# Performance work log

Measured on AMD Instinct MI355X. Metric: run time of the kernel, lower is better.

## Reference

```python
import jax, jax.numpy as jnp
import numpy as np
import math

B, CF, H, W = 2, 64, 256, 256
CH = 32          # 'channel' init arg
KS, DIL, PAD = 3, 2, 2
IMG_H, IMG_W = 512, 512


def _pos_encode(h, w, d_model):
    # Sinusoidal encoding along x and y, interleaved sin/cos -> [2*d_model, h, w]
    div = jnp.exp(jnp.arange(0, d_model, 2, dtype=jnp.float32) * (-math.log(10000.0) / d_model))  # [d/2]
    ax = jnp.arange(w, dtype=jnp.float32)[None, :] * div[:, None]   # [d/2, w]
    ay = jnp.arange(h, dtype=jnp.float32)[None, :] * div[:, None]   # [d/2, h]
    x = jnp.stack([jnp.sin(ax), jnp.cos(ax)], axis=1).reshape(d_model, w)  # even=sin, odd=cos
    y = jnp.stack([jnp.sin(ay), jnp.cos(ay)], axis=1).reshape(d_model, h)
    x = jnp.broadcast_to(x[:, None, :], (d_model, h, w))
    y = jnp.broadcast_to(y[:, :, None], (d_model, h, w))
    return jnp.concatenate([x, y], axis=0)  # [2*d_model, h, w]


def _unfold3x3(x):
    # F.unfold(kernel=3, dilation=2, padding=2, stride=1) -> [B, C, 9, H, W]
    b, c, h, w = x.shape
    xp = jnp.pad(x, ((0, 0), (0, 0), (PAD, PAD), (PAD, PAD)))
    offs = (0, DIL, 2 * DIL)
    patches = [xp[:, :, i:i + h, j:j + w] for i in offs for j in offs]  # row-major kernel order
    return jnp.stack(patches, axis=2)


def setup_inputs() -> dict:
    key = jax.random.key(0)
    k1, k2, k3, k4, k5 = jax.random.split(key, 5)
    return {
        "inp": jax.random.normal(k1, (B, CF, H, W), dtype=jnp.float32),
        "img": jax.random.uniform(k2, (B, 3, IMG_H, IMG_W), dtype=jnp.float32),
        "w_pos": jax.random.normal(k3, (CH, 2 * CH), dtype=jnp.float32) * 0.1,
        "w_img": jax.random.normal(k4, (CH, 3), dtype=jnp.float32) * 0.1,
        "w_comp": jax.random.normal(k5, (CF,), dtype=jnp.float32) * 0.1,
    }


def reference(inp, img, w_pos, w_img, w_comp):
    b, cf, h, w = inp.shape
    # positional embedding -> 1x1 conv (channel matmul)
    pos = _pos_encode(h, w, CH)                                   # [2*CH, H, W]
    pos_embd = jnp.einsum('oc,chw->ohw', w_pos, pos)              # [CH, H, W]
    pos_embd = jnp.broadcast_to(pos_embd[None], (b, CH, h, w))
    # bilinear resize of image to feature resolution, then 1x1 conv
    rimg = jax.image.resize(img, (b, 3, h, w), method='bilinear')
    rimg = jnp.einsum('oc,bchw->bohw', w_img, rimg)               # [B, CH, H, W]
    em = jnp.concatenate([rimg, pos_embd], axis=1)                # [B, 2*CH, H, W]
    # neighborhood similarity score
    un_em = _unfold3x3(em)                                        # [B, 2CH, 9, H, W]
    feature_score = jnp.einsum('bckhw,bchw->bkhw', un_em, em)     # [B, 9, H, W]
    # feature compatibility: 1x1 conv (dot with w_comp) per neighbor, sigmoid
    un_fea = _unfold3x3(inp)                                      # [B, CF, 9, H, W]
    comp_score = jax.nn.sigmoid(jnp.einsum('bckhw,c->bkhw', un_fea, w_comp))
    phi = comp_score * feature_score                              # [B, 9, H, W]
    weighted_fea = jnp.einsum('bckhw,bkhw->bchw', un_fea, phi)    # [B, CF, H, W]
    return weighted_fea
```

## Files before the change

kernel.cpp:

```cpp
#include <hip/hip_runtime.h>
#include <math.h>

namespace {
constexpr int Bn = 2, CF = 64;
constexpr int H = 256, W = 256, HW = H * W;
constexpr int IH = 512, IW = 512;

constexpr int OFF_MT   = 0;
constexpr int OFF_GXX  = OFF_MT + 256 * 256;
constexpr int OFF_GYY  = OFF_GXX + 3 * 256;
constexpr int OFF_G    = OFF_GYY + 3 * 256;
constexpr int OFF_RIMG = OFF_G + 16;
constexpr int OFF_S    = OFF_RIMG + Bn * 3 * HW;
constexpr int OFF_PHI  = OFF_S + Bn * HW;
constexpr int OFF_PX   = OFF_RIMG;
constexpr int OFF_PY   = OFF_RIMG + 32 * 256;
}

__global__ __launch_bounds__(256) void pxy_kernel(
    const float* __restrict__ w_pos,
    float* __restrict__ PX, float* __restrict__ PY)
{
  const int t = threadIdx.x;
  const int o = blockIdx.x;
  float s[16], c[16];
#pragma unroll
  for (int i = 0; i < 16; i++) {
    float d = expf((float)(2 * i) * (-0.2878231366242557f));
    float a = (float)t * d;
    s[i] = sinf(a);
    c[i] = cosf(a);
  }
  const float* wr = w_pos + o * 64;
  float ax = 0.f, ay = 0.f;
#pragma unroll
  for (int i = 0; i < 16; i++) {
    ax += wr[2 * i] * s[i] + wr[2 * i + 1] * c[i];
    ay += wr[32 + 2 * i] * s[i] + wr[33 + 2 * i] * c[i];
  }
  PX[o * 256 + t] = ax;
  PY[o * 256 + t] = ay;
}

__global__ __launch_bounds__(256) void gram_kernel(
    const float* __restrict__ PX, const float* __restrict__ PY,
    const float* __restrict__ w_img,
    float* __restrict__ Mt, float* __restrict__ GXX, float* __restrict__ GYY,
    float* __restrict__ G)
{
  const int a = threadIdx.x;
  const int t = blockIdx.x;

  float m = 0.f;
#pragma unroll
  for (int o = 0; o < 32; o++) m += PX[o * 256 + a] * PY[o * 256 + t];
  Mt[t * 256 + a] = m;

  if (t == 0) {
#pragma unroll
    for (int j = 0; j < 3; j++) {
      const int nb = a + 2 * (j - 1);
      float gx = 0.f, gy = 0.f;
      if (nb >= 0 && nb < 256) {
#pragma unroll
        for (int o = 0; o < 32; o++) {
          gx += PX[o * 256 + a] * PX[o * 256 + nb];
          gy += PY[o * 256 + a] * PY[o * 256 + nb];
        }
      }
      GXX[j * 256 + a] = gx;
      GYY[j * 256 + a] = gy;
    }
    if (a < 9) {
      const int i = a / 3, j = a % 3;
      float g = 0.f;
#pragma unroll
      for (int o = 0; o < 32; o++) g += w_img[o * 3 + i] * w_img[o * 3 + j];
      G[a] = g;
    }
  }
}

__device__ __forceinline__ void resize_taps(int p, int n, float w[4], int idx[4])
{
#pragma unroll
  for (int r = 0; r < 4; r++) {
    int q = 2 * p - 1 + r;
    idx[r] = min(max(q, 0), 2 * n - 1);
  }
  if (p == 0)          { w[0] = 0.f;        w[1] = 3.f / 7.f; w[2] = 3.f / 7.f; w[3] = 1.f / 7.f; }
  else if (p == n - 1) { w[0] = 1.f / 7.f;  w[1] = 3.f / 7.f; w[2] = 3.f / 7.f; w[3] = 0.f; }
  else                 { w[0] = 0.125f;     w[1] = 0.375f;    w[2] = 0.375f;    w[3] = 0.125f; }
}

__global__ __launch_bounds__(256) void rimg_kernel(
    const float* __restrict__ img, float* __restrict__ rimg)
{
  const int p = blockIdx.x * 256 + threadIdx.x;
  const int c = blockIdx.y;
  const int b = blockIdx.z;
  const int x = p & (W - 1);
  const int y = p >> 8;

  float wy[4], wx[4];
  int ry[4], rx[4];
  resize_taps(y, H, wy, ry);
  resize_taps(x, W, wx, rx);

  const float* ip = img + ((size_t)(b * 3 + c) * IH) * IW;
  float acc = 0.f;
#pragma unroll
  for (int r = 0; r < 4; r++) {
    const float* rowp = ip + ry[r] * IW;
    float rs = wx[0] * rowp[rx[0]] + wx[1] * rowp[rx[1]] +
               wx[2] * rowp[rx[2]] + wx[3] * rowp[rx[3]];
    acc += wy[r] * rs;
  }
  rimg[((size_t)(b * 3 + c)) * HW + p] = acc;
}

__global__ __launch_bounds__(256) void sigs_kernel(
    const float* __restrict__ inp, const float* __restrict__ w_comp,
    float* __restrict__ sigs)
{
  __shared__ float4 red[256];
  const int lane = threadIdx.x & 63;
  const int cg = threadIdx.x >> 6;
  const int p0 = blockIdx.x * 256 + lane * 4;
  const int b = blockIdx.z;

  const float* ib = inp + (size_t)b * CF * HW + (size_t)cg * 16 * HW + p0;
  float4 acc = {0.f, 0.f, 0.f, 0.f};
#pragma unroll
  for (int c = 0; c < 16; c++) {
    const float4 v = *reinterpret_cast<const float4*>(ib + (size_t)c * HW);
    const float wc = w_comp[cg * 16 + c];
    acc.x += v.x * wc; acc.y += v.y * wc;
    acc.z += v.z * wc; acc.w += v.w * wc;
  }
  red[threadIdx.x] = acc;
  __syncthreads();
  if (threadIdx.x < 64) {
    const float4 a = red[threadIdx.x];
    const float4 b1 = red[threadIdx.x + 64];
    const float4 c1 = red[threadIdx.x + 128];
    const float4 d = red[threadIdx.x + 192];
    float4 s;
    s.x = (a.x + b1.x) + (c1.x + d.x);
    s.y = (a.y + b1.y) + (c1.y + d.y);
    s.z = (a.z + b1.z) + (c1.z + d.z);
    s.w = (a.w + b1.w) + (c1.w + d.w);
    s.x = 1.f / (1.f + expf(-s.x));
    s.y = 1.f / (1.f + expf(-s.y));
    s.z = 1.f / (1.f + expf(-s.z));
    s.w = 1.f / (1.f + expf(-s.w));
    *reinterpret_cast<float4*>(sigs + (size_t)b * HW +
                               blockIdx.x * 256 + threadIdx.x * 4) = s;
  }
}

__global__ __launch_bounds__(256) void phi_kernel(
    const float* __restrict__ rimg, const float* __restrict__ sigs,
    const float* __restrict__ Mt, const float* __restrict__ GXX,
    const float* __restrict__ GYY, const float* __restrict__ G,
    float* __restrict__ phi)
{
  const int p = blockIdx.x * 256 + threadIdx.x;
  const int b = blockIdx.y;
  const int x = p & (W - 1);
  const int y = p >> 8;

  const float* rb = rimg + (size_t)b * 3 * HW;
  const float r0 = rb[p], r1 = rb[HW + p], r2 = rb[2 * HW + p];
  const float g0 = G[0], g1 = G[1], g2 = G[2];
  const float g3 = G[3], g4 = G[4], g5 = G[5];
  const float g6 = G[6], g7 = G[7], g8 = G[8];
  const float* sb = sigs + (size_t)b * HW;
  float* phb = phi + (size_t)b * 9 * HW;

#pragma unroll
  for (int k = 0; k < 9; k++) {
    const int ky = k / 3, kx = k % 3;
    const int ny = y + 2 * (ky - 1), nx = x + 2 * (kx - 1);
    const bool valid = ((unsigned)ny < (unsigned)H) & ((unsigned)nx < (unsigned)W);
    const int cy = min(max(ny, 0), H - 1);
    const int cx = min(max(nx, 0), W - 1);
    const int np = cy * W + cx;

    const float n0 = rb[np], n1 = rb[HW + np], n2 = rb[2 * HW + np];
    float fs = r0 * (g0 * n0 + g1 * n1 + g2 * n2)
             + r1 * (g3 * n0 + g4 * n1 + g5 * n2)
             + r2 * (g6 * n0 + g7 * n1 + g8 * n2);
    fs += GXX[kx * 256 + x] + GYY[ky * 256 + y]
        + Mt[y * 256 + cx] + Mt[cy * 256 + x];

    phb[(size_t)k * HW + p] = valid ? sb[np] * fs : 0.f;
  }
}

__global__ __launch_bounds__(256) void gather_kernel(
    const float* __restrict__ inp, const float* __restrict__ phi,
    float* __restrict__ out)
{
  const int tid = threadIdx.x;
  const int p0 = (blockIdx.y * 256 + tid) * 4;
  const int b = blockIdx.z;
  const int c0 = blockIdx.x * 8;
  const int x0 = p0 & (W - 1);
  const int y  = p0 >> 8;

  const float* phb = phi + (size_t)b * 9 * HW + p0;
  float4 ph[9];
#pragma unroll
  for (int k = 0; k < 9; k++)
    ph[k] = *reinterpret_cast<const float4*>(phb + (size_t)k * HW);

  const int xl = max(x0 - 4, 0);
  const int xr = min(x0 + 4, W - 4);
  int off[3][3];
#pragma unroll
  for (int ky = 0; ky < 3; ky++) {
    const int cy = min(max(y + 2 * (ky - 1), 0), H - 1);
    off[ky][0] = cy * W + xl;
    off[ky][1] = cy * W + x0;
    off[ky][2] = cy * W + xr;
  }

  const float* ib = inp + ((size_t)b * CF + c0) * HW;
  float* ob = out + ((size_t)b * CF + c0) * HW + p0;
#pragma unroll 2
  for (int c = 0; c < 8; c++) {
    const float* ic = ib + (size_t)c * HW;
    float4 acc = {0.f, 0.f, 0.f, 0.f};
#pragma unroll
    for (int ky = 0; ky < 3; ky++) {
      const float4 q0 = *reinterpret_cast<const float4*>(ic + off[ky][0]);
      const float4 q1 = *reinterpret_cast<const float4*>(ic + off[ky][1]);
      const float4 q2 = *reinterpret_cast<const float4*>(ic + off[ky][2]);
      const float a[12] = {q0.x, q0.y, q0.z, q0.w,
                           q1.x, q1.y, q1.z, q1.w,
                           q2.x, q2.y, q2.z, q2.w};
#pragma unroll
      for (int kx = 0; kx < 3; kx++) {
        const float4 w = ph[ky * 3 + kx];
        acc.x += w.x * a[2 + 2 * kx + 0];
        acc.y += w.y * a[2 + 2 * kx + 1];
        acc.z += w.z * a[2 + 2 * kx + 2];
        acc.w += w.w * a[2 + 2 * kx + 3];
      }
    }
    *reinterpret_cast<float4*>(ob + (size_t)c * HW) = acc;
  }
}

extern "C" void kernel_launch(void* const* d_in, const int* in_sizes, int n_in,
                              void* d_out, int out_size, void* d_ws, size_t ws_size,
                              hipStream_t stream)
{
  const float* inp    = (const float*)d_in[0];
  const float* img    = (const float*)d_in[1];
  const float* w_pos  = (const float*)d_in[2];
  const float* w_img  = (const float*)d_in[3];
  const float* w_comp = (const float*)d_in[4];
  float* out = (float*)d_out;
  float* ws  = (float*)d_ws;

  float* Mt   = ws + OFF_MT;
  float* GXX  = ws + OFF_GXX;
  float* GYY  = ws + OFF_GYY;
  float* G    = ws + OFF_G;
  float* rimg = ws + OFF_RIMG;
  float* sigs = ws + OFF_S;
  float* phi  = ws + OFF_PHI;
  float* PX   = ws + OFF_PX;
  float* PY   = ws + OFF_PY;

  hipLaunchKernelGGL(pxy_kernel, dim3(32), dim3(256), 0, stream, w_pos, PX, PY);
  hipLaunchKernelGGL(gram_kernel, dim3(256), dim3(256), 0, stream,
                     PX, PY, w_img, Mt, GXX, GYY, G);

  hipLaunchKernelGGL(rimg_kernel, dim3(HW / 256, 3, Bn), dim3(256), 0, stream,
                     img, rimg);
  hipLaunchKernelGGL(sigs_kernel, dim3(HW / 256, 1, Bn), dim3(256), 0, stream,
                     inp, w_comp, sigs);

  hipLaunchKernelGGL(phi_kernel, dim3(HW / 256, Bn), dim3(256), 0, stream,
                     rimg, sigs, Mt, GXX, GYY, G, phi);

  hipLaunchKernelGGL(gather_kernel, dim3(CF / 8, HW / 1024, Bn), dim3(256), 0, stream,
                     inp, phi, out);
}
```

Measured before the change: 135.8 us.

## Fuse phi computation into gather kernel and recompute phi per channel group

Removes the separate phi kernel and its 9-plane phi buffer. Each gather block now computes its nine neighbor weights in registers from rimg, sigs and the Gram tables, then applies them to 16 channels instead of 8. The halo loads shrink from three float4 per row to float2+float4+float2. This drops a launch and the phi write/read traffic, but phi is recomputed once per channel group (4 times) and register pressure rises.

```diff
diff --git a/kernel.cpp b/kernel.cpp
--- a/kernel.cpp
+++ b/kernel.cpp
@@ -12,7 +12,6 @@
 constexpr int OFF_G    = OFF_GYY + 3 * 256;
 constexpr int OFF_RIMG = OFF_G + 16;
 constexpr int OFF_S    = OFF_RIMG + Bn * 3 * HW;
-constexpr int OFF_PHI  = OFF_S + Bn * HW;
 constexpr int OFF_PX   = OFF_RIMG;
 constexpr int OFF_PY   = OFF_RIMG + 32 * 256;
 }
@@ -159,94 +158,153 @@
   }
 }
 
-__global__ __launch_bounds__(256) void phi_kernel(
-    const float* __restrict__ rimg, const float* __restrict__ sigs,
-    const float* __restrict__ Mt, const float* __restrict__ GXX,
-    const float* __restrict__ GYY, const float* __restrict__ G,
-    float* __restrict__ phi)
-{
-  const int p = blockIdx.x * 256 + threadIdx.x;
-  const int b = blockIdx.y;
-  const int x = p & (W - 1);
-  const int y = p >> 8;
-
-  const float* rb = rimg + (size_t)b * 3 * HW;
-  const float r0 = rb[p], r1 = rb[HW + p], r2 = rb[2 * HW + p];
-  const float g0 = G[0], g1 = G[1], g2 = G[2];
-  const float g3 = G[3], g4 = G[4], g5 = G[5];
-  const float g6 = G[6], g7 = G[7], g8 = G[8];
-  const float* sb = sigs + (size_t)b * HW;
-  float* phb = phi + (size_t)b * 9 * HW;
-
-#pragma unroll
-  for (int k = 0; k < 9; k++) {
-    const int ky = k / 3, kx = k % 3;
-    const int ny = y + 2 * (ky - 1), nx = x + 2 * (kx - 1);
-    const bool valid = ((unsigned)ny < (unsigned)H) & ((unsigned)nx < (unsigned)W);
-    const int cy = min(max(ny, 0), H - 1);
-    const int cx = min(max(nx, 0), W - 1);
-    const int np = cy * W + cx;
-
-    const float n0 = rb[np], n1 = rb[HW + np], n2 = rb[2 * HW + np];
-    float fs = r0 * (g0 * n0 + g1 * n1 + g2 * n2)
-             + r1 * (g3 * n0 + g4 * n1 + g5 * n2)
-             + r2 * (g6 * n0 + g7 * n1 + g8 * n2);
-    fs += GXX[kx * 256 + x] + GYY[ky * 256 + y]
-        + Mt[y * 256 + cx] + Mt[cy * 256 + x];
-
-    phb[(size_t)k * HW + p] = valid ? sb[np] * fs : 0.f;
-  }
-}
-
-__global__ __launch_bounds__(256) void gather_kernel(
-    const float* __restrict__ inp, const float* __restrict__ phi,
-    float* __restrict__ out)
-{
-  const int tid = threadIdx.x;
-  const int p0 = (blockIdx.y * 256 + tid) * 4;
+__global__ __launch_bounds__(256) void phigather_kernel(
+    const float* __restrict__ inp, const float* __restrict__ rimg,
+    const float* __restrict__ sigs, const float* __restrict__ Mt,
+    const float* __restrict__ GXX, const float* __restrict__ GYY,
+    const float* __restrict__ G, float* __restrict__ out)
+{
+  const int cg = blockIdx.x;
+  const int p0 = (blockIdx.y * 256 + threadIdx.x) * 4;
   const int b = blockIdx.z;
-  const int c0 = blockIdx.x * 8;
   const int x0 = p0 & (W - 1);
   const int y  = p0 >> 8;
 
-  const float* phb = phi + (size_t)b * 9 * HW + p0;
+  const int xl = max(x0 - 2, 0);
+  const int xr = min(x0 + 4, W - 2);
+
+  int rowoff[3];
+  bool vrow[3];
+#pragma unroll
+  for (int ky = 0; ky < 3; ky++) {
+    const int cy = y + 2 * (ky - 1);
+    vrow[ky] = ((unsigned)cy < (unsigned)H);
+    rowoff[ky] = min(max(cy, 0), H - 1) * W;
+  }
+
+  const float* rb = rimg + (size_t)b * 3 * HW;
+  const float* sb = sigs + (size_t)b * HW;
+
+  const float4 r0 = *reinterpret_cast<const float4*>(rb + p0);
+  const float4 r1 = *reinterpret_cast<const float4*>(rb + HW + p0);
+  const float4 r2 = *reinterpret_cast<const float4*>(rb + 2 * HW + p0);
+  float4 t0, t1, t2;
+  {
+    const float g0 = G[0], g1 = G[1], g2 = G[2];
+    const float g3 = G[3], g4 = G[4], g5 = G[5];
+    const float g6 = G[6], g7 = G[7], g8 = G[8];
+    t0.x = r0.x * g0 + r1.x * g3 + r2.x * g6;
+    t0.y = r0.y * g0 + r1.y * g3 + r2.y * g6;
+    t0.z = r0.z * g0 + r1.z * g3 + r2.z * g6;
+    t0.w = r0.w * g0 + r1.w * g3 + r2.w * g6;
+    t1.x = r0.x * g1 + r1.x * g4 + r2.x * g7;
+    t1.y = r0.y * g1 + r1.y * g4 + r2.y * g7;
+    t1.z = r0.z * g1 + r1.z * g4 + r2.z * g7;
+    t1.w = r0.w * g1 + r1.w * g4 + r2.w * g7;
+    t2.x = r0.x * g2 + r1.x * g5 + r2.x * g8;
+    t2.y = r0.y * g2 + r1.y * g5 + r2.y * g8;
+    t2.z = r0.z * g2 + r1.z * g5 + r2.z * g8;
+    t2.w = r0.w * g2 + r1.w * g5 + r2.w * g8;
+  }
+
+  float mrow[8];
+  {
+    const float2 L = *reinterpret_cast<const float2*>(Mt + y * W + xl);
+    const float4 C = *reinterpret_cast<const float4*>(Mt + y * W + x0);
+    const float2 R = *reinterpret_cast<const float2*>(Mt + y * W + xr);
+    mrow[0] = L.x; mrow[1] = L.y; mrow[2] = C.x; mrow[3] = C.y;
+    mrow[4] = C.z; mrow[5] = C.w; mrow[6] = R.x; mrow[7] = R.y;
+  }
+  float4 gxxv[3];
+#pragma unroll
+  for (int kx = 0; kx < 3; kx++)
+    gxxv[kx] = *reinterpret_cast<const float4*>(GXX + kx * 256 + x0);
+
   float4 ph[9];
 #pragma unroll
-  for (int k = 0; k < 9; k++)
-    ph[k] = *reinterpret_cast<const float4*>(phb + (size_t)k * HW);
-
-  const int xl = max(x0 - 4, 0);
-  const int xr = min(x0 + 4, W - 4);
-  int off[3][3];
-#pragma unroll
   for (int ky = 0; ky < 3; ky++) {
-    const int cy = min(max(y + 2 * (ky - 1), 0), H - 1);
-    off[ky][0] = cy * W + xl;
-    off[ky][1] = cy * W + x0;
-    off[ky][2] = cy * W + xr;
-  }
-
-  const float* ib = inp + ((size_t)b * CF + c0) * HW;
-  float* ob = out + ((size_t)b * CF + c0) * HW + p0;
-#pragma unroll 2
-  for (int c = 0; c < 8; c++) {
+    const int ro = rowoff[ky];
+    float a0[8], a1[8], a2[8], as_[8];
+    {
+      const float2 L0 = *reinterpret_cast<const float2*>(rb + ro + xl);
+      const float4 C0 = *reinterpret_cast<const float4*>(rb + ro + x0);
+      const float2 R0 = *reinterpret_cast<const float2*>(rb + ro + xr);
+      a0[0]=L0.x; a0[1]=L0.y; a0[2]=C0.x; a0[3]=C0.y;
+      a0[4]=C0.z; a0[5]=C0.w; a0[6]=R0.x; a0[7]=R0.y;
+      const float2 L1 = *reinterpret_cast<const float2*>(rb + HW + ro + xl);
+      const float4 C1 = *reinterpret_cast<const float4*>(rb + HW + ro + x0);
+      const float2 R1 = *reinterpret_cast<const float2*>(rb + HW + ro + xr);
+      a1[0]=L1.x; a1[1]=L1.y; a1[2]=C1.x; a1[3]=C1.y;
+      a1[4]=C1.z; a1[5]=C1.w; a1[6]=R1.x; a1[7]=R1.y;
+      const float2 L2 = *reinterpret_cast<const float2*>(rb + 2 * HW + ro + xl);
+      const float4 C2 = *reinterpret_cast<const float4*>(rb + 2 * HW + ro + x0);
+      const float2 R2 = *reinterpret_cast<const float2*>(rb + 2 * HW + ro + xr);
+      a2[0]=L2.x; a2[1]=L2.y; a2[2]=C2.x; a2[3]=C2.y;
+      a2[4]=C2.z; a2[5]=C2.w; a2[6]=R2.x; a2[7]=R2.y;
+      const float2 Ls = *reinterpret_cast<const float2*>(sb + ro + xl);
+      const float4 Cs = *reinterpret_cast<const float4*>(sb + ro + x0);
+      const float2 Rs = *reinterpret_cast<const float2*>(sb + ro + xr);
+      as_[0]=Ls.x; as_[1]=Ls.y; as_[2]=Cs.x; as_[3]=Cs.y;
+      as_[4]=Cs.z; as_[5]=Cs.w; as_[6]=Rs.x; as_[7]=Rs.y;
+    }
+    const float4 mc = *reinterpret_cast<const float4*>(Mt + ro + x0);
+    const float gyy = GYY[ky * 256 + y];
+
+#pragma unroll
+    for (int kx = 0; kx < 3; kx++) {
+      float4 p;
+      {
+        const int rel = 0 + 2 * kx;
+        const float fs = t0.x * a0[rel] + t1.x * a1[rel] + t2.x * a2[rel]
+                       + gxxv[kx].x + gyy + mrow[rel] + mc.x;
+        const bool v = vrow[ky] && ((unsigned)(x0 + 0 + 2 * (kx - 1)) < (unsigned)W);
+        p.x = v ? as_[rel] * fs : 0.f;
+      }
+      {
+        const int rel = 1 + 2 * kx;
+        const float fs = t0.y * a0[rel] + t1.y * a1[rel] + t2.y * a2[rel]
+                       + gxxv[kx].y + gyy + mrow[rel] + mc.y;
+        const bool v = vrow[ky] && ((unsigned)(x0 + 1 + 2 * (kx - 1)) < (unsigned)W);
+        p.y = v ? as_[rel] * fs : 0.f;
+      }
+      {
+        const int rel = 2 + 2 * kx;
+        const float fs = t0.z * a0[rel] + t1.z * a1[rel] + t2.z * a2[rel]
+                       + gxxv[kx].z + gyy + mrow[rel] + mc.z;
+        const bool v = vrow[ky] && ((unsigned)(x0 + 2 + 2 * (kx - 1)) < (unsigned)W);
+        p.z = v ? as_[rel] * fs : 0.f;
+      }
+      {
+        const int rel = 3 + 2 * kx;
+        const float fs = t0.w * a0[rel] + t1.w * a1[rel] + t2.w * a2[rel]
+                       + gxxv[kx].w + gyy + mrow[rel] + mc.w;
+        const bool v = vrow[ky] && ((unsigned)(x0 + 3 + 2 * (kx - 1)) < (unsigned)W);
+        p.w = v ? as_[rel] * fs : 0.f;
+      }
+      ph[ky * 3 + kx] = p;
+    }
+  }
+
+  const float* ib = inp + ((size_t)b * CF + cg * 16) * HW;
+  float* ob = out + ((size_t)b * CF + cg * 16) * HW + p0;
+#pragma unroll 4
+  for (int c = 0; c < 16; c++) {
     const float* ic = ib + (size_t)c * HW;
     float4 acc = {0.f, 0.f, 0.f, 0.f};
 #pragma unroll
     for (int ky = 0; ky < 3; ky++) {
-      const float4 q0 = *reinterpret_cast<const float4*>(ic + off[ky][0]);
-      const float4 q1 = *reinterpret_cast<const float4*>(ic + off[ky][1]);
-      const float4 q2 = *reinterpret_cast<const float4*>(ic + off[ky][2]);
-      const float a[12] = {q0.x, q0.y, q0.z, q0.w,
-                           q1.x, q1.y, q1.z, q1.w,
-                           q2.x, q2.y, q2.z, q2.w};
+      const int ro = rowoff[ky];
+      const float2 L = *reinterpret_cast<const float2*>(ic + ro + xl);
+      const float4 C = *reinterpret_cast<const float4*>(ic + ro + x0);
+      const float2 R = *reinterpret_cast<const float2*>(ic + ro + xr);
+      const float a[8] = {L.x, L.y, C.x, C.y, C.z, C.w, R.x, R.y};
 #pragma unroll
       for (int kx = 0; kx < 3; kx++) {
         const float4 w = ph[ky * 3 + kx];
-        acc.x += w.x * a[2 + 2 * kx + 0];
-        acc.y += w.y * a[2 + 2 * kx + 1];
-        acc.z += w.z * a[2 + 2 * kx + 2];
-        acc.w += w.w * a[2 + 2 * kx + 3];
+        acc.x += w.x * a[0 + 2 * kx];
+        acc.y += w.y * a[1 + 2 * kx];
+        acc.z += w.z * a[2 + 2 * kx];
+        acc.w += w.w * a[3 + 2 * kx];
       }
     }
     *reinterpret_cast<float4*>(ob + (size_t)c * HW) = acc;
@@ -271,7 +329,6 @@
   float* G    = ws + OFF_G;
   float* rimg = ws + OFF_RIMG;
   float* sigs = ws + OFF_S;
-  float* phi  = ws + OFF_PHI;
   float* PX   = ws + OFF_PX;
   float* PY   = ws + OFF_PY;
 
@@ -284,9 +341,6 @@
   hipLaunchKernelGGL(sigs_kernel, dim3(HW / 256, 1, Bn), dim3(256), 0, stream,
                      inp, w_comp, sigs);
 
-  hipLaunchKernelGGL(phi_kernel, dim3(HW / 256, Bn), dim3(256), 0, stream,
-                     rimg, sigs, Mt, GXX, GYY, G, phi);
-
-  hipLaunchKernelGGL(gather_kernel, dim3(CF / 8, HW / 1024, Bn), dim3(256), 0, stream,
-                     inp, phi, out);
-}
+  hipLaunchKernelGGL(phigather_kernel, dim3(CF / 16, HW / 1024, Bn), dim3(256), 0, stream,
+                     inp, rimg, sigs, Mt, GXX, GYY, G, out);
+}
```

After: 134.6 us. Within noise of the previous version (-0.9%).
